# Performance work log

Measured on AMD Instinct MI355X. Metric: run time of the kernel, lower is better.

Reference implementation:

```python
import jax, jax.numpy as jnp
import numpy as np

TEMPERATURE = 0.5
EPS = 1e-8  # torch CosineSimilarity eps


def setup_inputs() -> dict:
    key = jax.random.key(0)
    k1, k2 = jax.random.split(key)
    N, D = 4096, 256
    z1 = jax.random.normal(k1, (N, D), dtype=jnp.float32)
    z2 = jax.random.normal(k2, (N, D), dtype=jnp.float32)
    return {"z1": z1, "z2": z2}


def reference(z1, z2):
    N = z1.shape[0]
    z = jnp.concatenate([z1, z2], axis=0)  # [2N, D]
    # cosine similarity = normalized dot products (GEMM instead of O(N^2 D) broadcast)
    norm = jnp.linalg.norm(z, axis=-1, keepdims=True)
    zn = z / jnp.maximum(norm, EPS)
    sim = (zn @ zn.T) / TEMPERATURE  # [2N, 2N]
    # mask self-similarity on the diagonal
    idx = jnp.arange(2 * N)
    sim = jnp.where(idx[:, None] == idx[None, :], -jnp.inf, sim)
    # target[i] = (i - N) mod 2N  (arange(2N).roll(N))
    target = jnp.roll(idx, N)
    logp = jax.nn.log_softmax(sim, axis=-1)
    loss = -jnp.mean(logp[idx, target])
    return loss
```

## Files before the change

kernel.cpp:

```cpp
#include <hip/hip_runtime.h>

typedef __bf16 bf16x8 __attribute__((ext_vector_type(8)));
typedef float f32x4 __attribute__((ext_vector_type(4)));

#define TWO_LOG2E 2.88539008177792681f

#define GLOADLDS16(g, l) __builtin_amdgcn_global_load_lds(                     \
    (const __attribute__((address_space(1))) void*)(g),                        \
    (__attribute__((address_space(3))) void*)(l), 16, 0, 0)

__device__ __forceinline__ unsigned f2bf(float f) {
    unsigned u = __float_as_uint(f);
    return (u + 0x7FFFu + ((u >> 16) & 1u)) >> 16;
}

__global__ void __launch_bounds__(256) normalize_kernel(
    const float* __restrict__ z1, const float* __restrict__ z2,
    unsigned short* __restrict__ zn, float* __restrict__ S, float* __restrict__ out)
{
    if (blockIdx.x < 32) S[(blockIdx.x << 8) + threadIdx.x] = 0.f;
    if (blockIdx.x == 32 && threadIdx.x == 0) out[0] = 0.f;

    const int wave = threadIdx.x >> 6, lane = threadIdx.x & 63;
    const int row = (blockIdx.x << 2) + wave;
    const float* src = (row < 4096) ? (z1 + row * 256) : (z2 + (row - 4096) * 256);
    float4 v = ((const float4*)src)[lane];
    float ss = v.x * v.x + v.y * v.y + v.z * v.z + v.w * v.w;
#pragma unroll
    for (int m = 32; m > 0; m >>= 1) ss += __shfl_xor(ss, m, 64);
    float sc = 1.0f / fmaxf(sqrtf(ss), 1e-8f);
    uint2 w;
    w.x = f2bf(v.x * sc) | (f2bf(v.y * sc) << 16);
    w.y = f2bf(v.z * sc) | (f2bf(v.w * sc) << 16);
    *(uint2*)(zn + row * 256 + (lane << 2)) = w;
}

__global__ void __launch_bounds__(64, 2) simexp_kernel(
    const unsigned short* __restrict__ zn, float* __restrict__ S)
{
    __shared__ __align__(16) unsigned short Bs[4][2048];

    const int lane = threadIdx.x;
    const int q = lane >> 4, n16 = lane & 15;
    const int job = blockIdx.x;
    const int rowBase = (job >> 4) << 6;
    const int colRun  = (job & 15) << 9;

    bf16x8 a[4][8];
#pragma unroll
    for (int rt = 0; rt < 4; ++rt)
#pragma unroll
        for (int ks = 0; ks < 8; ++ks)
            a[rt][ks] = *(const bf16x8*)(zn + ((rowBase + (rt << 4) + n16) << 8)
                                            + (ks << 5) + (q << 3));

    auto stage = [&](int m, int off) {
        const int colBase = colRun + ((m >> 2) << 5);
        const int koff = (m & 3) << 6;
        unsigned short* base = (unsigned short*)&Bs[0][0] + off;
#pragma unroll
        for (int p = 0; p < 4; ++p) {
            int s = (p << 6) + lane;
            int c = s >> 3, d = s & 7;
            int k8 = d ^ (c & 7);
            GLOADLDS16(zn + ((colBase + c) << 8) + koff + (k8 << 3), base + (s << 3));
        }
    };

    float rs[4][4];
#pragma unroll
    for (int i = 0; i < 4; ++i)
#pragma unroll
        for (int j = 0; j < 4; ++j) rs[i][j] = 0.f;

    f32x4 acc[4][2];
    auto consume = [&](int off, int kc) {
        const unsigned short* bb = (const unsigned short*)&Bs[0][0] + off;
#pragma unroll
        for (int ks = 0; ks < 2; ++ks) {
            bf16x8 bf[2];
#pragma unroll
            for (int ct = 0; ct < 2; ++ct) {
                int c  = (ct << 4) + n16;
                int k8 = ((ks << 2) + q) ^ (c & 7);
                bf[ct] = *(const bf16x8*)(bb + (((c << 3) + k8) << 3));
            }
#pragma unroll
            for (int rt = 0; rt < 4; ++rt)
#pragma unroll
                for (int ct = 0; ct < 2; ++ct)
                    acc[rt][ct] = __builtin_amdgcn_mfma_f32_16x16x32_bf16(
                        a[rt][(kc << 1) + ks], bf[ct], acc[rt][ct], 0, 0, 0);
        }
    };
    auto epilogue = [&]() {
#pragma unroll
        for (int rt = 0; rt < 4; ++rt)
#pragma unroll
            for (int ct = 0; ct < 2; ++ct)
#pragma unroll
                for (int r = 0; r < 4; ++r)
                    rs[rt][r] += __builtin_amdgcn_exp2f(acc[rt][ct][r] * TWO_LOG2E);
    };

    stage(0, 0);
    stage(1, 2048);
    stage(2, 4096);
    int mp = 3;
    int off_p = 6144, off_c = 0;

    for (int cc = 0; cc < 15; ++cc) {
#pragma unroll
        for (int rt = 0; rt < 4; ++rt)
#pragma unroll
            for (int ct = 0; ct < 2; ++ct) acc[rt][ct] = (f32x4){0.f, 0.f, 0.f, 0.f};
#pragma unroll
        for (int kc = 0; kc < 4; ++kc) {
            stage(mp, off_p);
            asm volatile("s_waitcnt vmcnt(12)" ::: "memory");
            consume(off_c, kc);
            ++mp;
            off_p = (off_p + 2048) & 8191;
            off_c = (off_c + 2048) & 8191;
        }
        epilogue();
    }
#pragma unroll
    for (int rt = 0; rt < 4; ++rt)
#pragma unroll
        for (int ct = 0; ct < 2; ++ct) acc[rt][ct] = (f32x4){0.f, 0.f, 0.f, 0.f};
    stage(63, off_p);
    asm volatile("s_waitcnt vmcnt(12)" ::: "memory");
    consume(off_c, 0);
    off_c = (off_c + 2048) & 8191;
    asm volatile("s_waitcnt vmcnt(8)" ::: "memory");
    consume(off_c, 1);
    off_c = (off_c + 2048) & 8191;
    asm volatile("s_waitcnt vmcnt(4)" ::: "memory");
    consume(off_c, 2);
    off_c = (off_c + 2048) & 8191;
    asm volatile("s_waitcnt vmcnt(0)" ::: "memory");
    consume(off_c, 3);
    epilogue();

#pragma unroll
    for (int rt = 0; rt < 4; ++rt)
#pragma unroll
        for (int r = 0; r < 4; ++r) {
            float s = rs[rt][r];
            s += __shfl_xor(s, 1, 64);
            s += __shfl_xor(s, 2, 64);
            s += __shfl_xor(s, 4, 64);
            s += __shfl_xor(s, 8, 64);
            if (n16 == 0) atomicAdd(&S[rowBase + (rt << 4) + (q << 2) + r], s);
        }
}

__global__ void __launch_bounds__(256) finish_kernel(
    const unsigned short* __restrict__ zn, const float* __restrict__ S,
    float* __restrict__ out)
{
    __shared__ float vals[16];
    const int tid = threadIdx.x, lane = tid & 63, wave = tid >> 6;
    const int q = lane >> 4, n16 = lane & 15;
    const int rib = (wave << 2) + q;
    const int row = (blockIdx.x << 4) + rib;
    const int tar = (row + 4096) & 8191;

    float drr = 0.f, drt = 0.f;
#pragma unroll
    for (int i = 0; i < 4; ++i) {
        int k = (i << 6) + (n16 << 2);
        uint2 ur = *(const uint2*)(zn + (row << 8) + k);
        uint2 ut = *(const uint2*)(zn + (tar << 8) + k);
        float a0 = __uint_as_float(ur.x << 16),  a1 = __uint_as_float(ur.x & 0xFFFF0000u);
        float a2 = __uint_as_float(ur.y << 16),  a3 = __uint_as_float(ur.y & 0xFFFF0000u);
        float b0 = __uint_as_float(ut.x << 16),  b1 = __uint_as_float(ut.x & 0xFFFF0000u);
        float b2 = __uint_as_float(ut.y << 16),  b3 = __uint_as_float(ut.y & 0xFFFF0000u);
        drr += a0 * a0 + a1 * a1 + a2 * a2 + a3 * a3;
        drt += a0 * b0 + a1 * b1 + a2 * b2 + a3 * b3;
    }
#pragma unroll
    for (int m = 1; m <= 8; m <<= 1) {
        drr += __shfl_xor(drr, m, 64);
        drt += __shfl_xor(drt, m, 64);
    }
    if (n16 == 0) {
        float Sv = S[row] - __builtin_amdgcn_exp2f(drr * TWO_LOG2E);
        vals[rib] = 0.693147180559945f * __builtin_amdgcn_logf(Sv) - 2.0f * drt;
    }
    __syncthreads();
    if (tid == 0) {
        float s = 0.f;
#pragma unroll
        for (int i = 0; i < 16; ++i) s += vals[i];
        atomicAdd(out, s * (1.0f / 8192.0f));
    }
}

extern "C" void kernel_launch(void* const* d_in, const int* in_sizes, int n_in,
                              void* d_out, int out_size, void* d_ws, size_t ws_size,
                              hipStream_t stream)
{
    const float* z1 = (const float*)d_in[0];
    const float* z2 = (const float*)d_in[1];
    unsigned short* zn = (unsigned short*)d_ws;
    float* S = (float*)((char*)d_ws + 8192 * 256 * sizeof(unsigned short));
    float* out = (float*)d_out;

    normalize_kernel<<<2048, 256, 0, stream>>>(z1, z2, zn, S, out);
    simexp_kernel<<<2048, 64, 0, stream>>>(zn, S);
    finish_kernel<<<512, 256, 0, stream>>>(zn, S, out);
}
```

Measured before the change: 105.2 us.

## Share staged B tiles across four waves per block in simexp kernel

The similarity-exp kernel moves from one wave per block covering 64 rows to four waves per block covering 128 rows, 32 rows per wave. All four waves share one LDS ring of B column tiles. Each wave now stages one 16-byte slice per step instead of four, and block barriers replace the per-wave vmcnt-only pipeline. This halves the global/L2 reads of the B matrix per output row and reduces per-wave A-register footprint, which may raise occupancy. In exchange it adds a barrier per k-step, shortens the prefetch distance to two, and lowers the MFMA work per LDS read within each wave.

```diff
diff --git a/kernel.cpp b/kernel.cpp
--- a/kernel.cpp
+++ b/kernel.cpp
@@ -35,47 +35,46 @@
     *(uint2*)(zn + row * 256 + (lane << 2)) = w;
 }
 
-__global__ void __launch_bounds__(64, 2) simexp_kernel(
+__global__ void __launch_bounds__(256, 4) simexp_kernel(
     const unsigned short* __restrict__ zn, float* __restrict__ S)
 {
     __shared__ __align__(16) unsigned short Bs[4][2048];
 
-    const int lane = threadIdx.x;
+    const int tid = threadIdx.x;
+    const int wv = tid >> 6, lane = tid & 63;
     const int q = lane >> 4, n16 = lane & 15;
     const int job = blockIdx.x;
-    const int rowBase = (job >> 4) << 6;
+    const int rowBase = (job >> 4) << 7;
     const int colRun  = (job & 15) << 9;
-
-    bf16x8 a[4][8];
-#pragma unroll
-    for (int rt = 0; rt < 4; ++rt)
+    const int rowW = rowBase + (wv << 5);
+
+    bf16x8 a[2][8];
+#pragma unroll
+    for (int rt = 0; rt < 2; ++rt)
 #pragma unroll
         for (int ks = 0; ks < 8; ++ks)
-            a[rt][ks] = *(const bf16x8*)(zn + ((rowBase + (rt << 4) + n16) << 8)
+            a[rt][ks] = *(const bf16x8*)(zn + ((rowW + (rt << 4) + n16) << 8)
                                             + (ks << 5) + (q << 3));
 
-    auto stage = [&](int m, int off) {
+    auto stage = [&](int m) {
         const int colBase = colRun + ((m >> 2) << 5);
         const int koff = (m & 3) << 6;
-        unsigned short* base = (unsigned short*)&Bs[0][0] + off;
-#pragma unroll
-        for (int p = 0; p < 4; ++p) {
-            int s = (p << 6) + lane;
-            int c = s >> 3, d = s & 7;
-            int k8 = d ^ (c & 7);
-            GLOADLDS16(zn + ((colBase + c) << 8) + koff + (k8 << 3), base + (s << 3));
-        }
-    };
-
-    float rs[4][4];
-#pragma unroll
-    for (int i = 0; i < 4; ++i)
+        unsigned short* base = &Bs[m & 3][0];
+        int s = (wv << 6) + lane;
+        int c = s >> 3, d = s & 7;
+        int k8 = d ^ (c & 7);
+        GLOADLDS16(zn + ((colBase + c) << 8) + koff + (k8 << 3), base + (s << 3));
+    };
+
+    float rs[2][4];
+#pragma unroll
+    for (int i = 0; i < 2; ++i)
 #pragma unroll
         for (int j = 0; j < 4; ++j) rs[i][j] = 0.f;
 
-    f32x4 acc[4][2];
-    auto consume = [&](int off, int kc) {
-        const unsigned short* bb = (const unsigned short*)&Bs[0][0] + off;
+    f32x4 acc[2][2];
+    auto consume = [&](int kc) {
+        const unsigned short* bb = &Bs[kc & 3][0];
 #pragma unroll
         for (int ks = 0; ks < 2; ++ks) {
             bf16x8 bf[2];
@@ -86,16 +85,22 @@
                 bf[ct] = *(const bf16x8*)(bb + (((c << 3) + k8) << 3));
             }
 #pragma unroll
-            for (int rt = 0; rt < 4; ++rt)
+            for (int rt = 0; rt < 2; ++rt)
 #pragma unroll
                 for (int ct = 0; ct < 2; ++ct)
                     acc[rt][ct] = __builtin_amdgcn_mfma_f32_16x16x32_bf16(
                         a[rt][(kc << 1) + ks], bf[ct], acc[rt][ct], 0, 0, 0);
         }
     };
+    auto zacc = [&]() {
+#pragma unroll
+        for (int rt = 0; rt < 2; ++rt)
+#pragma unroll
+            for (int ct = 0; ct < 2; ++ct) acc[rt][ct] = (f32x4){0.f, 0.f, 0.f, 0.f};
+    };
     auto epilogue = [&]() {
 #pragma unroll
-        for (int rt = 0; rt < 4; ++rt)
+        for (int rt = 0; rt < 2; ++rt)
 #pragma unroll
             for (int ct = 0; ct < 2; ++ct)
 #pragma unroll
@@ -103,48 +108,44 @@
                     rs[rt][r] += __builtin_amdgcn_exp2f(acc[rt][ct][r] * TWO_LOG2E);
     };
 
-    stage(0, 0);
-    stage(1, 2048);
-    stage(2, 4096);
-    int mp = 3;
-    int off_p = 6144, off_c = 0;
+    stage(0);
+    stage(1);
 
     for (int cc = 0; cc < 15; ++cc) {
-#pragma unroll
-        for (int rt = 0; rt < 4; ++rt)
-#pragma unroll
-            for (int ct = 0; ct < 2; ++ct) acc[rt][ct] = (f32x4){0.f, 0.f, 0.f, 0.f};
+        zacc();
 #pragma unroll
         for (int kc = 0; kc < 4; ++kc) {
-            stage(mp, off_p);
-            asm volatile("s_waitcnt vmcnt(12)" ::: "memory");
-            consume(off_c, kc);
-            ++mp;
-            off_p = (off_p + 2048) & 8191;
-            off_c = (off_c + 2048) & 8191;
+            stage((cc << 2) + kc + 2);
+            asm volatile("s_waitcnt vmcnt(2)" ::: "memory");
+            __builtin_amdgcn_s_barrier();
+            asm volatile("" ::: "memory");
+            consume(kc);
         }
         epilogue();
     }
-#pragma unroll
-    for (int rt = 0; rt < 4; ++rt)
-#pragma unroll
-        for (int ct = 0; ct < 2; ++ct) acc[rt][ct] = (f32x4){0.f, 0.f, 0.f, 0.f};
-    stage(63, off_p);
-    asm volatile("s_waitcnt vmcnt(12)" ::: "memory");
-    consume(off_c, 0);
-    off_c = (off_c + 2048) & 8191;
-    asm volatile("s_waitcnt vmcnt(8)" ::: "memory");
-    consume(off_c, 1);
-    off_c = (off_c + 2048) & 8191;
-    asm volatile("s_waitcnt vmcnt(4)" ::: "memory");
-    consume(off_c, 2);
-    off_c = (off_c + 2048) & 8191;
+    zacc();
+    stage(62);
+    asm volatile("s_waitcnt vmcnt(2)" ::: "memory");
+    __builtin_amdgcn_s_barrier();
+    asm volatile("" ::: "memory");
+    consume(0);
+    stage(63);
+    asm volatile("s_waitcnt vmcnt(2)" ::: "memory");
+    __builtin_amdgcn_s_barrier();
+    asm volatile("" ::: "memory");
+    consume(1);
+    asm volatile("s_waitcnt vmcnt(1)" ::: "memory");
+    __builtin_amdgcn_s_barrier();
+    asm volatile("" ::: "memory");
+    consume(2);
     asm volatile("s_waitcnt vmcnt(0)" ::: "memory");
-    consume(off_c, 3);
+    __builtin_amdgcn_s_barrier();
+    asm volatile("" ::: "memory");
+    consume(3);
     epilogue();
 
 #pragma unroll
-    for (int rt = 0; rt < 4; ++rt)
+    for (int rt = 0; rt < 2; ++rt)
 #pragma unroll
         for (int r = 0; r < 4; ++r) {
             float s = rs[rt][r];
@@ -152,7 +153,7 @@
             s += __shfl_xor(s, 2, 64);
             s += __shfl_xor(s, 4, 64);
             s += __shfl_xor(s, 8, 64);
-            if (n16 == 0) atomicAdd(&S[rowBase + (rt << 4) + (q << 2) + r], s);
+            if (n16 == 0) atomicAdd(&S[rowW + (rt << 4) + (q << 2) + r], s);
         }
 }
 
@@ -209,6 +210,6 @@
     float* out = (float*)d_out;
 
     normalize_kernel<<<2048, 256, 0, stream>>>(z1, z2, zn, S, out);
-    simexp_kernel<<<2048, 64, 0, stream>>>(zn, S);
+    simexp_kernel<<<1024, 256, 0, stream>>>(zn, S);
     finish_kernel<<<512, 256, 0, stream>>>(zn, S, out);
 }
```

After: 104.4 us. About the same (-0.7%).

## Exploit symmetry of similarity matrix by computing only upper-triangular tiles

Applied to the files above, without the earlier changes.

Because the similarity matrix is symmetric, each block now computes only tiles on or above the diagonal and adds its exponentials into both the row sums and the column sums. Diagonal-straddling tiles are masked so each pair is counted once and the diagonal only in the row sum. The column sums go to S through extra cross-lane reductions and atomics. This roughly halves the MFMA and exp work, at the cost of more atomics, uneven work across blocks and an index decode loop at block start.

```diff
diff --git a/kernel.cpp b/kernel.cpp
--- a/kernel.cpp
+++ b/kernel.cpp
@@ -42,9 +42,16 @@
 
     const int lane = threadIdx.x;
     const int q = lane >> 4, n16 = lane & 15;
-    const int job = blockIdx.x;
-    const int rowBase = (job >> 4) << 6;
-    const int colRun  = (job & 15) << 9;
+
+    const int job = 2111 - blockIdx.x;
+    int c2 = 0, rem = job;
+    while (rem >= (c2 << 2) + 4) { rem -= (c2 << 2) + 4; ++c2; }
+    const int r = rem;
+    const int k = r - (c2 << 2);
+    const bool straddle = (k >= 0);
+    const int cc0 = straddle ? (k << 1) : 0;
+    const int rowBase = r << 6;
+    const int colRun  = c2 << 8;
 
     bf16x8 a[4][8];
 #pragma unroll
@@ -54,10 +61,10 @@
             a[rt][ks] = *(const bf16x8*)(zn + ((rowBase + (rt << 4) + n16) << 8)
                                             + (ks << 5) + (q << 3));
 
-    auto stage = [&](int m, int off) {
+    auto stage = [&](int m) {
         const int colBase = colRun + ((m >> 2) << 5);
         const int koff = (m & 3) << 6;
-        unsigned short* base = (unsigned short*)&Bs[0][0] + off;
+        unsigned short* base = &Bs[m & 3][0];
 #pragma unroll
         for (int p = 0; p < 4; ++p) {
             int s = (p << 6) + lane;
@@ -74,8 +81,8 @@
         for (int j = 0; j < 4; ++j) rs[i][j] = 0.f;
 
     f32x4 acc[4][2];
-    auto consume = [&](int off, int kc) {
-        const unsigned short* bb = (const unsigned short*)&Bs[0][0] + off;
+    auto consume = [&](int kc) {
+        const unsigned short* bb = &Bs[kc][0];
 #pragma unroll
         for (int ks = 0; ks < 2; ++ks) {
             bf16x8 bf[2];
@@ -93,66 +100,79 @@
                         a[rt][(kc << 1) + ks], bf[ct], acc[rt][ct], 0, 0, 0);
         }
     };
-    auto epilogue = [&]() {
+    auto zacc = [&]() {
 #pragma unroll
         for (int rt = 0; rt < 4; ++rt)
 #pragma unroll
-            for (int ct = 0; ct < 2; ++ct)
-#pragma unroll
-                for (int r = 0; r < 4; ++r)
-                    rs[rt][r] += __builtin_amdgcn_exp2f(acc[rt][ct][r] * TWO_LOG2E);
-    };
-
-    stage(0, 0);
-    stage(1, 2048);
-    stage(2, 4096);
-    int mp = 3;
-    int off_p = 6144, off_c = 0;
-
-    for (int cc = 0; cc < 15; ++cc) {
+            for (int ct = 0; ct < 2; ++ct) acc[rt][ct] = (f32x4){0.f, 0.f, 0.f, 0.f};
+    };
+    auto epiC = [&](int cc, bool msk) {
+        float cs[2] = {0.f, 0.f};
+        const int colC = colRun + (cc << 5);
 #pragma unroll
         for (int rt = 0; rt < 4; ++rt)
 #pragma unroll
-            for (int ct = 0; ct < 2; ++ct) acc[rt][ct] = (f32x4){0.f, 0.f, 0.f, 0.f};
+            for (int ct = 0; ct < 2; ++ct) {
+                const int col = colC + (ct << 4) + n16;
+                const int rw0 = rowBase + (rt << 4) + (q << 2);
+#pragma unroll
+                for (int rr = 0; rr < 4; ++rr) {
+                    float e = __builtin_amdgcn_exp2f(acc[rt][ct][rr] * TWO_LOG2E);
+                    if (msk) {
+                        int row = rw0 + rr;
+                        rs[rt][rr] += (col >= row) ? e : 0.f;
+                        cs[ct]     += (col >  row) ? e : 0.f;
+                    } else {
+                        rs[rt][rr] += e;
+                        cs[ct] += e;
+                    }
+                }
+            }
+#pragma unroll
+        for (int ct = 0; ct < 2; ++ct) {
+            float s = cs[ct];
+            s += __shfl_xor(s, 16, 64);
+            s += __shfl_xor(s, 32, 64);
+            if (lane < 16) atomicAdd(&S[colC + (ct << 4) + n16], s);
+        }
+    };
+
+    const int m0 = cc0 << 2;
+    stage(m0); stage(m0 + 1); stage(m0 + 2);
+
+    for (int cc = cc0; cc < 7; ++cc) {
+        zacc();
+        const bool msk = straddle && (cc < (k << 1) + 2);
 #pragma unroll
         for (int kc = 0; kc < 4; ++kc) {
-            stage(mp, off_p);
+            stage((cc << 2) + kc + 3);
             asm volatile("s_waitcnt vmcnt(12)" ::: "memory");
-            consume(off_c, kc);
-            ++mp;
-            off_p = (off_p + 2048) & 8191;
-            off_c = (off_c + 2048) & 8191;
-        }
-        epilogue();
-    }
+            consume(kc);
+        }
+        epiC(cc, msk);
+    }
+    zacc();
+    stage(31);
+    asm volatile("s_waitcnt vmcnt(12)" ::: "memory");
+    consume(0);
+    asm volatile("s_waitcnt vmcnt(8)" ::: "memory");
+    consume(1);
+    asm volatile("s_waitcnt vmcnt(4)" ::: "memory");
+    consume(2);
+    asm volatile("s_waitcnt vmcnt(0)" ::: "memory");
+    consume(3);
+    epiC(7, straddle && (7 < (k << 1) + 2));
+
 #pragma unroll
     for (int rt = 0; rt < 4; ++rt)
 #pragma unroll
-        for (int ct = 0; ct < 2; ++ct) acc[rt][ct] = (f32x4){0.f, 0.f, 0.f, 0.f};
-    stage(63, off_p);
-    asm volatile("s_waitcnt vmcnt(12)" ::: "memory");
-    consume(off_c, 0);
-    off_c = (off_c + 2048) & 8191;
-    asm volatile("s_waitcnt vmcnt(8)" ::: "memory");
-    consume(off_c, 1);
-    off_c = (off_c + 2048) & 8191;
-    asm volatile("s_waitcnt vmcnt(4)" ::: "memory");
-    consume(off_c, 2);
-    off_c = (off_c + 2048) & 8191;
-    asm volatile("s_waitcnt vmcnt(0)" ::: "memory");
-    consume(off_c, 3);
-    epilogue();
-
-#pragma unroll
-    for (int rt = 0; rt < 4; ++rt)
-#pragma unroll
-        for (int r = 0; r < 4; ++r) {
-            float s = rs[rt][r];
+        for (int rr = 0; rr < 4; ++rr) {
+            float s = rs[rt][rr];
             s += __shfl_xor(s, 1, 64);
             s += __shfl_xor(s, 2, 64);
             s += __shfl_xor(s, 4, 64);
             s += __shfl_xor(s, 8, 64);
-            if (n16 == 0) atomicAdd(&S[rowBase + (rt << 4) + (q << 2) + r], s);
+            if (n16 == 0) atomicAdd(&S[rowBase + (rt << 4) + (q << 2) + rr], s);
         }
 }
 
@@ -209,6 +229,6 @@
     float* out = (float*)d_out;
 
     normalize_kernel<<<2048, 256, 0, stream>>>(z1, z2, zn, S, out);
-    simexp_kernel<<<2048, 64, 0, stream>>>(zn, S);
+    simexp_kernel<<<2112, 64, 0, stream>>>(zn, S);
     finish_kernel<<<512, 256, 0, stream>>>(zn, S, out);
 }
```

Result: slower. 114.6 us (+8.9%).
